# Optimization experiments

Hardware: AMD Instinct MI355X
Metric: run time of the kernel (lower is better)

Reference implementation:

```python
import jax, jax.numpy as jnp
import numpy as np

B, S, D, H, DH, CACHE = 2, 2048, 1024, 16, 64, 2048
MAX_KV = 4096
F16_MAX = 65504.0  # tf.float16.max, used as the additive mask penalty in the original


def setup_inputs() -> dict:
    key = jax.random.key(0)
    ks = jax.random.split(key, 9)
    s = 0.02
    return {
        "q": jax.random.normal(ks[0], (B, S, D), jnp.float32),
        "k": jax.random.normal(ks[1], (B, S, D), jnp.float32),
        "v": jax.random.normal(ks[2], (B, S, D), jnp.float32),
        "cache_k": jax.random.normal(ks[3], (B, 1, CACHE, DH), jnp.float32),
        "cache_v": jax.random.normal(ks[4], (B, 1, CACHE, DH), jnp.float32),
        "wq": jax.random.normal(ks[5], (D, H * DH), jnp.float32) * s,
        "wk": jax.random.normal(ks[6], (D, DH), jnp.float32) * s,
        "wv": jax.random.normal(ks[7], (D, DH), jnp.float32) * s,
        "wo": jax.random.normal(ks[8], (H * DH, D), jnp.float32) * s,
    }


def reference(q, k, v, cache_k, cache_v, wq, wk, wv, wo):
    scale = 1.0 / np.sqrt(DH).astype(np.float32)
    b, s = q.shape[0], q.shape[1]
    # projections
    qh = (q @ wq).reshape(b, s, H, DH).transpose(0, 2, 1, 3)        # [B,H,S,dh]
    kh = (k @ wk).reshape(b, s, 1, DH).transpose(0, 2, 1, 3)        # [B,1,S,dh]
    vh = (v @ wv).reshape(b, s, 1, DH).transpose(0, 2, 1, 3)        # [B,1,S,dh]
    # KV cache concat + truncate to max_kv_length
    kc = jnp.concatenate([cache_k, kh], axis=2)[:, :, -MAX_KV:, :]  # [B,1,K,dh]
    vc = jnp.concatenate([cache_v, vh], axis=2)[:, :, -MAX_KV:, :]
    kk = kc[:, 0]  # [B,K,dh]  (single shared KV head)
    vv = vc[:, 0]
    # scores: [B,H,S,K]
    scores = jnp.einsum("bhqd,bkd->bhqk", qh, kk) * scale
    # causal mask exactly as tf.linalg.band_part(ones, -1, 0): mask[i,j] = j <= i
    klen = kk.shape[1]
    causal = jnp.tril(jnp.ones((s, klen), bool))                    # [S,K]
    scores = scores - (1.0 - causal.astype(scores.dtype)) * F16_MAX
    att = jax.nn.softmax(scores, axis=-1)
    vals = jnp.einsum("bhqk,bkd->bhqd", att, vv)                    # [B,H,S,dh]
    vals = vals.transpose(0, 2, 1, 3).reshape(b, s, H * DH)
    out = vals @ wo                                                 # [B,S,D]
    return out, kc, vc
```

## Files before the change

### kernel.cpp

```cpp
#include <hip/hip_runtime.h>
#include <hip/hip_bf16.h>
#include <type_traits>

#define B_ 2
#define S_ 2048
#define D_ 1024
#define H_ 16
#define DH_ 64
#define CACHE_ 2048
#define MAXKV_ 4096

using f32x4  = __attribute__((ext_vector_type(4))) float;
using bf16x8 = __attribute__((ext_vector_type(8))) short;
using bf16x4 = __attribute__((ext_vector_type(4))) short;

__device__ inline short f2bf(float x) {
  __hip_bfloat16 h = __float2bfloat16(x);
  short r;
  __builtin_memcpy(&r, &h, 2);
  return r;
}
__device__ inline void stor(float* p, float x) { *p = x; }
__device__ inline void stor(__hip_bfloat16* p, float x) { *p = __float2bfloat16(x); }

__device__ inline void glds16(const short* g, short* l) {
  __builtin_amdgcn_global_load_lds(
      (const __attribute__((address_space(1))) void*)g,
      (__attribute__((address_space(3))) void*)l, 16, 0, 0);
}

__device__ inline void tile_transpose(const float* __restrict__ in,
                                      short* __restrict__ out, int R, int C,
                                      int r0, int c0, int t, float T[64][65]) {
#pragma unroll
  for (int p = 0; p < 16; ++p) {
    int li = t + p * 256;
    int r = li >> 6, c = li & 63;
    T[r][c] = in[(size_t)(r0 + r) * C + c0 + c];
  }
  __syncthreads();
#pragma unroll
  for (int p = 0; p < 16; ++p) {
    int li = t + p * 256;
    int c = li >> 6, r = li & 63;
    out[(size_t)(c0 + c) * R + r0 + r] = f2bf(T[r][c]);
  }
}

__global__ __launch_bounds__(256) void prep_kernel(
    const float* __restrict__ q, const float* __restrict__ ck,
    const float* __restrict__ cv, const float* __restrict__ wq,
    const float* __restrict__ wk, const float* __restrict__ wv,
    const float* __restrict__ wo, short* __restrict__ qbf,
    float4* __restrict__ kc, float4* __restrict__ vc,
    short* __restrict__ ckbf, short* __restrict__ cvT,
    short* __restrict__ wqT, short* __restrict__ wkT,
    short* __restrict__ wvT, short* __restrict__ woT) {
  __shared__ float T[64][65];
  const int bx = blockIdx.x, t = threadIdx.x;
  if (bx < 1024) {
    int base = bx * 4096 + t * 4;
#pragma unroll
    for (int p = 0; p < 4; ++p) {
      int i = base + p * 1024;
      float4 f = *(const float4*)&q[i];
      bf16x4 s;
      s[0] = f2bf(f.x); s[1] = f2bf(f.y); s[2] = f2bf(f.z); s[3] = f2bf(f.w);
      *(bf16x4*)&qbf[i] = s;
    }
  } else if (bx < 1280) {
    int idx = (bx - 1024) * 256 + t;
    const int per_b = CACHE_ * DH_ / 4;
    int b = idx / per_b, rem = idx % per_b;
    int dst = b * (MAXKV_ * DH_ / 4) + rem;
    float4 a = ((const float4*)ck)[idx], c = ((const float4*)cv)[idx];
    kc[dst] = a;
    vc[dst] = c;
    bf16x4 s;
    s[0] = f2bf(a.x); s[1] = f2bf(a.y); s[2] = f2bf(a.z); s[3] = f2bf(a.w);
    *(bf16x4*)&ckbf[idx * 4] = s;
  } else if (bx < 1344) {
    int tt = bx - 1280;
    int b = tt >> 5, tile = tt & 31;
    tile_transpose(cv + (size_t)b * CACHE_ * DH_, cvT + (size_t)b * DH_ * CACHE_,
                   CACHE_, DH_, tile * 64, 0, t, T);
  } else if (bx < 1856) {
    int tt = bx - 1344;
    int sel = tt >> 8;
    tt &= 255;
    tile_transpose(sel ? wo : wq, sel ? woT : wqT, D_, D_, (tt >> 4) * 64,
                   (tt & 15) * 64, t, T);
  } else {
    int tt = bx - 1856;
    int sel = tt >> 4, tile = tt & 15;
    tile_transpose(sel ? wv : wk, sel ? wvT : wkT, D_, DH_, tile * 64, 0, t, T);
  }
}

__global__ __launch_bounds__(256) void gemm_kv(
    const float* __restrict__ A, const short* __restrict__ Bt,
    float* __restrict__ C, int K, const float* __restrict__ A2,
    const short* __restrict__ Bt2, float* __restrict__ C2) {
  if (blockIdx.z) { A = A2; Bt = Bt2; C = C2; }
  __shared__ __align__(16) short As[32 * 40];
  __shared__ __align__(16) short Bs[64 * 40];
  const int t = threadIdx.x;
  const int w = t >> 6, lane = t & 63, lx = lane & 15, quad = lane >> 4;
  const int row_base = (w & 1) * 16, col_base = (w >> 1) * 32;
  const int row0 = blockIdx.x * 32;

  f32x4 acc[2];
  acc[0] = (f32x4){0.f, 0.f, 0.f, 0.f};
  acc[1] = (f32x4){0.f, 0.f, 0.f, 0.f};

  for (int k0 = 0; k0 < K; k0 += 32) {
    {
      int row = t >> 3, kk0 = (t & 7) * 4;
      float4 f = *(const float4*)&A[(size_t)(row0 + row) * K + k0 + kk0];
      bf16x4 s;
      s[0] = f2bf(f.x); s[1] = f2bf(f.y); s[2] = f2bf(f.z); s[3] = f2bf(f.w);
      *(bf16x4*)&As[row * 40 + kk0] = s;
    }
    {
      int row = t >> 2, kk0 = (t & 3) * 8;
      *(bf16x8*)&Bs[row * 40 + kk0] =
          *(const bf16x8*)&Bt[(size_t)row * K + k0 + kk0];
    }
    __syncthreads();
    bf16x8 a = *(bf16x8*)&As[(row_base + lx) * 40 + quad * 8];
#pragma unroll
    for (int cb = 0; cb < 2; ++cb) {
      bf16x8 b = *(bf16x8*)&Bs[(col_base + cb * 16 + lx) * 40 + quad * 8];
      acc[cb] = __builtin_amdgcn_mfma_f32_16x16x32_bf16(a, b, acc[cb], 0, 0, 0);
    }
    __syncthreads();
  }

#pragma unroll
  for (int cb = 0; cb < 2; ++cb)
#pragma unroll
    for (int reg = 0; reg < 4; ++reg) {
      int r = row0 + row_base + quad * 4 + reg;
      int c = col_base + cb * 16 + lx;
      int bb = r >> 11, s = r & 2047;
      C[(size_t)bb * (MAXKV_ * DH_) + (size_t)(CACHE_ + s) * DH_ + c] =
          acc[cb][reg];
    }
}

template <typename TC>
__global__ __launch_bounds__(256) void gemm_glds(
    const short* __restrict__ A, const short* __restrict__ Bt,
    TC* __restrict__ C, int M, int N, int K, float scale) {
  __shared__ __align__(16) short As[128 * 32];
  __shared__ __align__(16) short Bs[64 * 32];
  const int t = threadIdx.x;
  const int w = t >> 6, lane = t & 63, lx = lane & 15, quad = lane >> 4;
  const int row0 = blockIdx.x * 128, col0 = blockIdx.y * 64;
  const int row_base = (w >> 1) * 64, col_base = (w & 1) * 32;

  const short* Ag = A + (size_t)(row0 + w * 32 + (lane >> 2)) * K + (lane & 3) * 8;
  const short* Bg = Bt + (size_t)(col0 + w * 16 + (lane >> 2)) * K + (lane & 3) * 8;
  short* Al = &As[(w * 32) * 32];
  short* Bl = &Bs[(w * 16) * 32];

  f32x4 acc[4][2];
#pragma unroll
  for (int mb = 0; mb < 4; ++mb)
#pragma unroll
    for (int cb = 0; cb < 2; ++cb) acc[mb][cb] = (f32x4){0.f, 0.f, 0.f, 0.f};

  for (int k0 = 0; k0 < K; k0 += 32) {
    glds16(Ag + k0, Al);
    glds16(Ag + 16 * K + k0, Al + 16 * 32);
    glds16(Bg + k0, Bl);
    __syncthreads();
    bf16x8 a[4], b[2];
#pragma unroll
    for (int mb = 0; mb < 4; ++mb)
      a[mb] = *(bf16x8*)&As[(row_base + mb * 16 + lx) * 32 + quad * 8];
#pragma unroll
    for (int cb = 0; cb < 2; ++cb)
      b[cb] = *(bf16x8*)&Bs[(col_base + cb * 16 + lx) * 32 + quad * 8];
#pragma unroll
    for (int mb = 0; mb < 4; ++mb)
#pragma unroll
      for (int cb = 0; cb < 2; ++cb)
        acc[mb][cb] = __builtin_amdgcn_mfma_f32_16x16x32_bf16(
            a[mb], b[cb], acc[mb][cb], 0, 0, 0);
    __syncthreads();
  }

#pragma unroll
  for (int mb = 0; mb < 4; ++mb)
#pragma unroll
    for (int cb = 0; cb < 2; ++cb)
#pragma unroll
      for (int reg = 0; reg < 4; ++reg) {
        int r = row0 + row_base + mb * 16 + quad * 4 + reg;
        int c = col0 + col_base + cb * 16 + lx;
        stor(&C[(size_t)r * N + c], acc[mb][cb][reg] * scale);
      }
}

__global__ __launch_bounds__(256) void attention_mfma(
    __hip_bfloat16* __restrict__ qh,
    const short* __restrict__ ckbf,
    const short* __restrict__ cvT) {
  __shared__ __align__(16) short Ks[64 * 72];
  __shared__ __align__(16) short Vt[64 * 72];
  __shared__ __align__(16) short Ps[64 * 72];
  const int t = threadIdx.x;
  const int w = t >> 6, lane = t & 63, lx = lane & 15, quad = lane >> 4;
  const int p = blockIdx.x, bh = blockIdx.y;
  const int b = bh >> 4, h = bh & 15;
  const int qtA = p, qtB = 31 - p;
  const int q0A = qtA * 64, q0B = qtB * 64;
  short* qhp = (short*)qh;

  bf16x8 aqA[2], aqB[2];
#pragma unroll
  for (int kb = 0; kb < 2; ++kb) {
    aqA[kb] = *(const bf16x8*)&qhp[(size_t)(b * S_ + q0A + w * 16 + lx) * (H_ * DH_) +
                                   h * DH_ + kb * 32 + quad * 8];
    aqB[kb] = *(const bf16x8*)&qhp[(size_t)(b * S_ + q0B + w * 16 + lx) * (H_ * DH_) +
                                   h * DH_ + kb * 32 + quad * 8];
  }

  f32x4 oA[4], oB[4];
#pragma unroll
  for (int d = 0; d < 4; ++d) {
    oA[d] = (f32x4){0.f, 0.f, 0.f, 0.f};
    oB[d] = (f32x4){0.f, 0.f, 0.f, 0.f};
  }
  float lA[4] = {0.f, 0.f, 0.f, 0.f}, lB[4] = {0.f, 0.f, 0.f, 0.f};

  for (int kt = 0; kt <= qtB; ++kt) {
    const int k0 = kt * 64;
#pragma unroll
    for (int pp = 0; pp < 2; ++pp) {
      int li = t + pp * 256;
      int row = li >> 3, kk0 = (li & 7) * 8;
      *(bf16x8*)&Ks[row * 72 + kk0] =
          *(const bf16x8*)&ckbf[(size_t)(b * CACHE_ + k0 + row) * DH_ + kk0];
      *(bf16x8*)&Vt[row * 72 + kk0] =
          *(const bf16x8*)&cvT[(size_t)(b * DH_ + row) * CACHE_ + k0 + kk0];
    }
    __syncthreads();

    {
      f32x4 accs[4];
#pragma unroll
      for (int cb = 0; cb < 4; ++cb) accs[cb] = (f32x4){0.f, 0.f, 0.f, 0.f};
#pragma unroll
      for (int cb = 0; cb < 4; ++cb)
#pragma unroll
        for (int kb = 0; kb < 2; ++kb) {
          bf16x8 bk = *(bf16x8*)&Ks[(cb * 16 + lx) * 72 + kb * 32 + quad * 8];
          accs[cb] = __builtin_amdgcn_mfma_f32_16x16x32_bf16(aqB[kb], bk, accs[cb], 0, 0, 0);
        }
      const bool diag = (kt == qtB);
#pragma unroll
      for (int cb = 0; cb < 4; ++cb)
#pragma unroll
        for (int reg = 0; reg < 4; ++reg) {
          float x = accs[cb][reg];
          if (diag && (cb * 16 + lx > w * 16 + quad * 4 + reg)) x = -1e30f;
          float pe = __expf(x - 10.0f);
          Ps[(w * 16 + quad * 4 + reg) * 72 + cb * 16 + lx] = f2bf(pe);
          lB[reg] += pe;
        }
#pragma unroll
      for (int kb = 0; kb < 2; ++kb) {
        bf16x8 ap = *(bf16x8*)&Ps[(w * 16 + lx) * 72 + kb * 32 + quad * 8];
#pragma unroll
        for (int d = 0; d < 4; ++d) {
          bf16x8 bv = *(bf16x8*)&Vt[(d * 16 + lx) * 72 + kb * 32 + quad * 8];
          oB[d] = __builtin_amdgcn_mfma_f32_16x16x32_bf16(ap, bv, oB[d], 0, 0, 0);
        }
      }
    }

    if (kt <= qtA) {
      f32x4 accs[4];
#pragma unroll
      for (int cb = 0; cb < 4; ++cb) accs[cb] = (f32x4){0.f, 0.f, 0.f, 0.f};
#pragma unroll
      for (int cb = 0; cb < 4; ++cb)
#pragma unroll
        for (int kb = 0; kb < 2; ++kb) {
          bf16x8 bk = *(bf16x8*)&Ks[(cb * 16 + lx) * 72 + kb * 32 + quad * 8];
          accs[cb] = __builtin_amdgcn_mfma_f32_16x16x32_bf16(aqA[kb], bk, accs[cb], 0, 0, 0);
        }
      const bool diag = (kt == qtA);
#pragma unroll
      for (int cb = 0; cb < 4; ++cb)
#pragma unroll
        for (int reg = 0; reg < 4; ++reg) {
          float x = accs[cb][reg];
          if (diag && (cb * 16 + lx > w * 16 + quad * 4 + reg)) x = -1e30f;
          float pe = __expf(x - 10.0f);
          Ps[(w * 16 + quad * 4 + reg) * 72 + cb * 16 + lx] = f2bf(pe);
          lA[reg] += pe;
        }
#pragma unroll
      for (int kb = 0; kb < 2; ++kb) {
        bf16x8 ap = *(bf16x8*)&Ps[(w * 16 + lx) * 72 + kb * 32 + quad * 8];
#pragma unroll
        for (int d = 0; d < 4; ++d) {
          bf16x8 bv = *(bf16x8*)&Vt[(d * 16 + lx) * 72 + kb * 32 + quad * 8];
          oA[d] = __builtin_amdgcn_mfma_f32_16x16x32_bf16(ap, bv, oA[d], 0, 0, 0);
        }
      }
    }
    __syncthreads();
  }

#pragma unroll
  for (int off = 1; off < 16; off <<= 1)
#pragma unroll
    for (int reg = 0; reg < 4; ++reg) {
      lA[reg] += __shfl_xor(lA[reg], off, 64);
      lB[reg] += __shfl_xor(lB[reg], off, 64);
    }

#pragma unroll
  for (int d = 0; d < 4; ++d)
#pragma unroll
    for (int reg = 0; reg < 4; ++reg) {
      int col = h * DH_ + d * 16 + lx;
      int qA = q0A + w * 16 + quad * 4 + reg;
      int qB = q0B + w * 16 + quad * 4 + reg;
      qhp[(size_t)(b * S_ + qA) * (H_ * DH_) + col] = f2bf(oA[d][reg] / lA[reg]);
      qhp[(size_t)(b * S_ + qB) * (H_ * DH_) + col] = f2bf(oB[d][reg] / lB[reg]);
    }
}

extern "C" void kernel_launch(void* const* d_in, const int* in_sizes, int n_in,
                              void* d_out, int out_size, void* d_ws, size_t ws_size,
                              hipStream_t stream) {
  const float* q  = (const float*)d_in[0];
  const float* k  = (const float*)d_in[1];
  const float* v  = (const float*)d_in[2];
  const float* ck = (const float*)d_in[3];
  const float* cv = (const float*)d_in[4];
  const float* wq = (const float*)d_in[5];
  const float* wk = (const float*)d_in[6];
  const float* wv = (const float*)d_in[7];
  const float* wo = (const float*)d_in[8];

  float* out = (float*)d_out;
  float* kc  = out + (size_t)B_ * S_ * D_;
  float* vc  = kc + (size_t)B_ * MAXKV_ * DH_;

  short* qbf = (short*)d_out;

  short* ws   = (short*)d_ws;
  short* qh   = ws;
  short* ckbf = qh + (size_t)B_ * S_ * H_ * DH_;
  short* cvT  = ckbf + (size_t)B_ * CACHE_ * DH_;
  short* wqT  = cvT + (size_t)B_ * CACHE_ * DH_;
  short* wkT  = wqT + (size_t)D_ * H_ * DH_;
  short* wvT  = wkT + (size_t)D_ * DH_;
  short* woT  = wvT + (size_t)D_ * DH_;

  prep_kernel<<<1888, 256, 0, stream>>>(q, ck, cv, wq, wk, wv, wo, qbf,
                                        (float4*)kc, (float4*)vc, ckbf, cvT,
                                        wqT, wkT, wvT, woT);
  gemm_kv<<<dim3(128, 1, 2), 256, 0, stream>>>(k, wkT, kc, D_, v, wvT, vc);
  gemm_glds<__hip_bfloat16><<<dim3(32, 16), 256, 0, stream>>>(
      qbf, wqT, (__hip_bfloat16*)qh, B_ * S_, H_ * DH_, D_, 0.125f);
  attention_mfma<<<dim3(16, B_ * H_), 256, 0, stream>>>(
      (__hip_bfloat16*)qh, ckbf, cvT);
  gemm_glds<float><<<dim3(32, 16), 256, 0, stream>>>(
      qh, woT, out, B_ * S_, D_, D_, 1.0f);
}
```

Before: 220.7 us.

## Deepen GEMM K-steps to 64 and hoist K/V fragments in attention

The KV projection GEMM and the glds GEMM now consume 64 K-elements per iteration instead of 32. This halves the number of barrier pairs and loop iterations, with larger or doubled shared-memory tiles. The attention kernel loads the K and V shared-memory fragments into registers once per key tile and reuses them for both query sub-tiles, rather than re-reading LDS for each. This raises register pressure, which may reduce occupancy.

```diff
diff --git a/kernel.cpp b/kernel.cpp
--- a/kernel.cpp
+++ b/kernel.cpp
@@ -102,8 +102,8 @@
     float* __restrict__ C, int K, const float* __restrict__ A2,
     const short* __restrict__ Bt2, float* __restrict__ C2) {
   if (blockIdx.z) { A = A2; Bt = Bt2; C = C2; }
-  __shared__ __align__(16) short As[32 * 40];
-  __shared__ __align__(16) short Bs[64 * 40];
+  __shared__ __align__(16) short As[32 * 72];
+  __shared__ __align__(16) short Bs[64 * 72];
   const int t = threadIdx.x;
   const int w = t >> 6, lane = t & 63, lx = lane & 15, quad = lane >> 4;
   const int row_base = (w & 1) * 16, col_base = (w >> 1) * 32;
@@ -113,25 +113,33 @@
   acc[0] = (f32x4){0.f, 0.f, 0.f, 0.f};
   acc[1] = (f32x4){0.f, 0.f, 0.f, 0.f};
 
-  for (int k0 = 0; k0 < K; k0 += 32) {
+  for (int k0 = 0; k0 < K; k0 += 64) {
     {
-      int row = t >> 3, kk0 = (t & 7) * 4;
-      float4 f = *(const float4*)&A[(size_t)(row0 + row) * K + k0 + kk0];
-      bf16x4 s;
-      s[0] = f2bf(f.x); s[1] = f2bf(f.y); s[2] = f2bf(f.z); s[3] = f2bf(f.w);
-      *(bf16x4*)&As[row * 40 + kk0] = s;
+      int row = t >> 3, c0 = (t & 7) * 8;
+      const float* src = &A[(size_t)(row0 + row) * K + k0 + c0];
+      float4 f0 = *(const float4*)src;
+      float4 f1 = *(const float4*)(src + 4);
+      bf16x4 s0, s1;
+      s0[0] = f2bf(f0.x); s0[1] = f2bf(f0.y); s0[2] = f2bf(f0.z); s0[3] = f2bf(f0.w);
+      s1[0] = f2bf(f1.x); s1[1] = f2bf(f1.y); s1[2] = f2bf(f1.z); s1[3] = f2bf(f1.w);
+      *(bf16x4*)&As[row * 72 + c0] = s0;
+      *(bf16x4*)&As[row * 72 + c0 + 4] = s1;
     }
     {
-      int row = t >> 2, kk0 = (t & 3) * 8;
-      *(bf16x8*)&Bs[row * 40 + kk0] =
-          *(const bf16x8*)&Bt[(size_t)row * K + k0 + kk0];
-    }
-    __syncthreads();
-    bf16x8 a = *(bf16x8*)&As[(row_base + lx) * 40 + quad * 8];
-#pragma unroll
-    for (int cb = 0; cb < 2; ++cb) {
-      bf16x8 b = *(bf16x8*)&Bs[(col_base + cb * 16 + lx) * 40 + quad * 8];
-      acc[cb] = __builtin_amdgcn_mfma_f32_16x16x32_bf16(a, b, acc[cb], 0, 0, 0);
+      int row = t >> 2, c0 = (t & 3) * 16;
+      const short* src = &Bt[(size_t)row * K + k0 + c0];
+      *(bf16x8*)&Bs[row * 72 + c0] = *(const bf16x8*)src;
+      *(bf16x8*)&Bs[row * 72 + c0 + 8] = *(const bf16x8*)(src + 8);
+    }
+    __syncthreads();
+#pragma unroll
+    for (int kb = 0; kb < 2; ++kb) {
+      bf16x8 a = *(bf16x8*)&As[(row_base + lx) * 72 + kb * 32 + quad * 8];
+#pragma unroll
+      for (int cb = 0; cb < 2; ++cb) {
+        bf16x8 b = *(bf16x8*)&Bs[(col_base + cb * 16 + lx) * 72 + kb * 32 + quad * 8];
+        acc[cb] = __builtin_amdgcn_mfma_f32_16x16x32_bf16(a, b, acc[cb], 0, 0, 0);
+      }
     }
     __syncthreads();
   }
@@ -152,8 +160,8 @@
 __global__ __launch_bounds__(256) void gemm_glds(
     const short* __restrict__ A, const short* __restrict__ Bt,
     TC* __restrict__ C, int M, int N, int K, float scale) {
-  __shared__ __align__(16) short As[128 * 32];
-  __shared__ __align__(16) short Bs[64 * 32];
+  __shared__ __align__(16) short As[2][128 * 32];
+  __shared__ __align__(16) short Bs[2][64 * 32];
   const int t = threadIdx.x;
   const int w = t >> 6, lane = t & 63, lx = lane & 15, quad = lane >> 4;
   const int row0 = blockIdx.x * 128, col0 = blockIdx.y * 64;
@@ -161,8 +169,10 @@
 
   const short* Ag = A + (size_t)(row0 + w * 32 + (lane >> 2)) * K + (lane & 3) * 8;
   const short* Bg = Bt + (size_t)(col0 + w * 16 + (lane >> 2)) * K + (lane & 3) * 8;
-  short* Al = &As[(w * 32) * 32];
-  short* Bl = &Bs[(w * 16) * 32];
+  short* Al0 = &As[0][(w * 32) * 32];
+  short* Al1 = &As[1][(w * 32) * 32];
+  short* Bl0 = &Bs[0][(w * 16) * 32];
+  short* Bl1 = &Bs[1][(w * 16) * 32];
 
   f32x4 acc[4][2];
 #pragma unroll
@@ -170,24 +180,33 @@
 #pragma unroll
     for (int cb = 0; cb < 2; ++cb) acc[mb][cb] = (f32x4){0.f, 0.f, 0.f, 0.f};
 
-  for (int k0 = 0; k0 < K; k0 += 32) {
-    glds16(Ag + k0, Al);
-    glds16(Ag + 16 * K + k0, Al + 16 * 32);
-    glds16(Bg + k0, Bl);
-    __syncthreads();
-    bf16x8 a[4], b[2];
+  for (int k0 = 0; k0 < K; k0 += 64) {
+    glds16(Ag + k0, Al0);
+    glds16(Ag + 16 * K + k0, Al0 + 16 * 32);
+    glds16(Ag + k0 + 32, Al1);
+    glds16(Ag + 16 * K + k0 + 32, Al1 + 16 * 32);
+    glds16(Bg + k0, Bl0);
+    glds16(Bg + k0 + 32, Bl1);
+    __syncthreads();
+    bf16x8 a[4][2], b[2][2];
 #pragma unroll
     for (int mb = 0; mb < 4; ++mb)
-      a[mb] = *(bf16x8*)&As[(row_base + mb * 16 + lx) * 32 + quad * 8];
+#pragma unroll
+      for (int kb = 0; kb < 2; ++kb)
+        a[mb][kb] = *(bf16x8*)&As[kb][(row_base + mb * 16 + lx) * 32 + quad * 8];
 #pragma unroll
     for (int cb = 0; cb < 2; ++cb)
-      b[cb] = *(bf16x8*)&Bs[(col_base + cb * 16 + lx) * 32 + quad * 8];
-#pragma unroll
-    for (int mb = 0; mb < 4; ++mb)
-#pragma unroll
-      for (int cb = 0; cb < 2; ++cb)
-        acc[mb][cb] = __builtin_amdgcn_mfma_f32_16x16x32_bf16(
-            a[mb], b[cb], acc[mb][cb], 0, 0, 0);
+#pragma unroll
+      for (int kb = 0; kb < 2; ++kb)
+        b[cb][kb] = *(bf16x8*)&Bs[kb][(col_base + cb * 16 + lx) * 32 + quad * 8];
+#pragma unroll
+    for (int kb = 0; kb < 2; ++kb)
+#pragma unroll
+      for (int mb = 0; mb < 4; ++mb)
+#pragma unroll
+        for (int cb = 0; cb < 2; ++cb)
+          acc[mb][cb] = __builtin_amdgcn_mfma_f32_16x16x32_bf16(
+              a[mb][kb], b[cb][kb], acc[mb][cb], 0, 0, 0);
     __syncthreads();
   }
 
@@ -248,6 +267,15 @@
     }
     __syncthreads();
 
+    bf16x8 bk[4][2], bv[4][2];
+#pragma unroll
+    for (int cb = 0; cb < 4; ++cb)
+#pragma unroll
+      for (int kb = 0; kb < 2; ++kb) {
+        bk[cb][kb] = *(bf16x8*)&Ks[(cb * 16 + lx) * 72 + kb * 32 + quad * 8];
+        bv[cb][kb] = *(bf16x8*)&Vt[(cb * 16 + lx) * 72 + kb * 32 + quad * 8];
+      }
+
     {
       f32x4 accs[4];
 #pragma unroll
@@ -255,10 +283,9 @@
 #pragma unroll
       for (int cb = 0; cb < 4; ++cb)
 #pragma unroll
-        for (int kb = 0; kb < 2; ++kb) {
-          bf16x8 bk = *(bf16x8*)&Ks[(cb * 16 + lx) * 72 + kb * 32 + quad * 8];
-          accs[cb] = __builtin_amdgcn_mfma_f32_16x16x32_bf16(aqB[kb], bk, accs[cb], 0, 0, 0);
-        }
+        for (int kb = 0; kb < 2; ++kb)
+          accs[cb] = __builtin_amdgcn_mfma_f32_16x16x32_bf16(aqB[kb], bk[cb][kb],
+                                                             accs[cb], 0, 0, 0);
       const bool diag = (kt == qtB);
 #pragma unroll
       for (int cb = 0; cb < 4; ++cb)
@@ -274,10 +301,8 @@
       for (int kb = 0; kb < 2; ++kb) {
         bf16x8 ap = *(bf16x8*)&Ps[(w * 16 + lx) * 72 + kb * 32 + quad * 8];
 #pragma unroll
-        for (int d = 0; d < 4; ++d) {
-          bf16x8 bv = *(bf16x8*)&Vt[(d * 16 + lx) * 72 + kb * 32 + quad * 8];
-          oB[d] = __builtin_amdgcn_mfma_f32_16x16x32_bf16(ap, bv, oB[d], 0, 0, 0);
-        }
+        for (int d = 0; d < 4; ++d)
+          oB[d] = __builtin_amdgcn_mfma_f32_16x16x32_bf16(ap, bv[d][kb], oB[d], 0, 0, 0);
       }
     }
 
@@ -288,10 +313,9 @@
 #pragma unroll
       for (int cb = 0; cb < 4; ++cb)
 #pragma unroll
-        for (int kb = 0; kb < 2; ++kb) {
-          bf16x8 bk = *(bf16x8*)&Ks[(cb * 16 + lx) * 72 + kb * 32 + quad * 8];
-          accs[cb] = __builtin_amdgcn_mfma_f32_16x16x32_bf16(aqA[kb], bk, accs[cb], 0, 0, 0);
-        }
+        for (int kb = 0; kb < 2; ++kb)
+          accs[cb] = __builtin_amdgcn_mfma_f32_16x16x32_bf16(aqA[kb], bk[cb][kb],
+                                                             accs[cb], 0, 0, 0);
       const bool diag = (kt == qtA);
 #pragma unroll
       for (int cb = 0; cb < 4; ++cb)
@@ -307,10 +331,8 @@
       for (int kb = 0; kb < 2; ++kb) {
         bf16x8 ap = *(bf16x8*)&Ps[(w * 16 + lx) * 72 + kb * 32 + quad * 8];
 #pragma unroll
-        for (int d = 0; d < 4; ++d) {
-          bf16x8 bv = *(bf16x8*)&Vt[(d * 16 + lx) * 72 + kb * 32 + quad * 8];
-          oA[d] = __builtin_amdgcn_mfma_f32_16x16x32_bf16(ap, bv, oA[d], 0, 0, 0);
-        }
+        for (int d = 0; d < 4; ++d)
+          oA[d] = __builtin_amdgcn_mfma_f32_16x16x32_bf16(ap, bv[d][kb], oA[d], 0, 0, 0);
       }
     }
     __syncthreads();
```

Result: faster. 209.4 us (-5.1%).
